# Kernel optimization log

Measured on AMD Instinct MI355X. Metric: run time of the kernel, lower is better.

## Reference

```python
import jax, jax.numpy as jnp
import numpy as np

D_K = 64  # per-head dim; source hardcodes d_k for the 1/sqrt(d_k) scale


def setup_inputs() -> dict:
    key = jax.random.key(0)
    kq, kk, kv = jax.random.split(key, 3)
    shape = (4, 16, 2048, D_K)  # [B, H, S, d]
    return {
        "q_s": jax.random.normal(kq, shape, dtype=jnp.float32),
        "k_s": jax.random.normal(kk, shape, dtype=jnp.float32),
        "v_s": jax.random.normal(kv, shape, dtype=jnp.float32),
    }


def reference(q_s, k_s, v_s):
    # scores = Q K^T / sqrt(d_k)  -> [B, H, S, S] (full matrix, unfused, as in source)
    scale = 1.0 / jnp.sqrt(jnp.asarray(D_K, dtype=q_s.dtype))
    scores = jnp.einsum("bhqd,bhkd->bhqk", q_s, k_s) * scale
    attn = jax.nn.softmax(scores, axis=-1)
    # out = attn @ V -> [B, H, S, d]
    return jnp.einsum("bhqk,bhkd->bhqd", attn, v_s)
```

## Files before the change

### kernel.cpp

```cpp
#include <hip/hip_runtime.h>
#include <stdint.h>
#include <math.h>

#define S_LEN 2048
#define DIM   64
#define QBLK  128
#define KVBLK 32
#define NKV   (S_LEN / KVBLK)

typedef __attribute__((ext_vector_type(8))) short short8;
typedef __attribute__((ext_vector_type(4))) float f32x4;

static __device__ __forceinline__ unsigned short f2bf(float f) {
    union { float f; uint32_t u; } cv; cv.f = f;
    uint32_t u = cv.u;
    return (unsigned short)((u + 0x7fffu + ((u >> 16) & 1u)) >> 16);
}

static __device__ __forceinline__ void gload16(const void* g, void* l) {
    __builtin_amdgcn_global_load_lds(
        (const __attribute__((address_space(1))) unsigned int*)g,
        (__attribute__((address_space(3))) unsigned int*)l, 16, 0, 0);
}

static __device__ __forceinline__ float vmax3(float a, float b, float c) {
    float d;
    asm("v_max3_f32 %0, %1, %2, %3" : "=v"(d) : "v"(a), "v"(b), "v"(c));
    return d;
}

__global__ void cvt_k(const float* __restrict__ kp, unsigned short* __restrict__ kws) {
    const int idx = blockIdx.x * 256 + threadIdx.x;
    const int c   = idx & 7;
    const int s   = (idx >> 3) & (S_LEN - 1);
    const int bh  = idx >> 14;
    const float* src = kp + ((size_t)bh * S_LEN + s) * DIM + c * 8;
    const f32x4 a = *reinterpret_cast<const f32x4*>(src);
    const f32x4 b = *reinterpret_cast<const f32x4*>(src + 4);
    short8 t;
    t[0] = (short)f2bf(a[0]); t[1] = (short)f2bf(a[1]);
    t[2] = (short)f2bf(a[2]); t[3] = (short)f2bf(a[3]);
    t[4] = (short)f2bf(b[0]); t[5] = (short)f2bf(b[1]);
    t[6] = (short)f2bf(b[2]); t[7] = (short)f2bf(b[3]);
    unsigned short* dst = kws + ((size_t)bh * S_LEN + s) * DIM + (size_t)((c ^ (s & 7)) * 8);
    *reinterpret_cast<short8*>(dst) = t;
}

__global__ void cvt_v(const float* __restrict__ vp, unsigned short* __restrict__ vtws) {
    const int bh = blockIdx.x >> 5;
    const int T  = blockIdx.x & 31;
    const int tid = threadIdx.x;
    __shared__ unsigned short ldsT[DIM][72];

    const int i = tid >> 2;
    const int dbase = (tid & 3) * 16;
    const float* src = vp + ((size_t)bh * S_LEN + T * 64 + i) * DIM + dbase;
#pragma unroll
    for (int q4 = 0; q4 < 4; ++q4) {
        const f32x4 a = *reinterpret_cast<const f32x4*>(src + q4 * 4);
#pragma unroll
        for (int j = 0; j < 4; ++j) ldsT[dbase + q4 * 4 + j][i] = f2bf(a[j]);
    }
    __syncthreads();
#pragma unroll
    for (int hh = 0; hh < 2; ++hh) {
        const int slot = tid + hh * 256;
        const int d = slot >> 3;
        const int h = (slot >> 2) & 1;
        const int c_st = slot & 3;
        const int cl = c_st ^ ((d >> 1) & 3);
        short8 t8;
#pragma unroll
        for (int j = 0; j < 8; ++j) {
            const int p = cl * 8 + j;
            const int kap = ((p & 4) << 2) | ((p & 16) >> 1) | ((p & 8) >> 1) | (p & 3);
            t8[j] = (short)ldsT[d][h * 32 + kap];
        }
        unsigned short* dst = vtws + ((size_t)bh * DIM + d) * S_LEN + T * 64 + h * 32 + c_st * 8;
        *reinterpret_cast<short8*>(dst) = t8;
    }
}

#define QK_TILE(ST, KL)                                                                               \
    do {                                                                                              \
        __builtin_amdgcn_s_setprio(1);                                                                \
        _Pragma("unroll")                                                                             \
        for (int nt = 0; nt < 2; ++nt) {                                                              \
            const short8 kf0 = *reinterpret_cast<const short8*>((KL) + koff[nt][0]);                  \
            const short8 kf1 = *reinterpret_cast<const short8*>((KL) + koff[nt][1]);                  \
            ST[0][nt] = __builtin_amdgcn_mfma_f32_16x16x32_bf16(kf0, qfrag[0][0], z4, 0, 0, 0);       \
            ST[1][nt] = __builtin_amdgcn_mfma_f32_16x16x32_bf16(kf0, qfrag[1][0], z4, 0, 0, 0);       \
            ST[0][nt] = __builtin_amdgcn_mfma_f32_16x16x32_bf16(kf1, qfrag[0][1], ST[0][nt], 0, 0, 0);\
            ST[1][nt] = __builtin_amdgcn_mfma_f32_16x16x32_bf16(kf1, qfrag[1][1], ST[1][nt], 0, 0, 0);\
        }                                                                                             \
        __builtin_amdgcn_s_setprio(0);                                                                \
    } while (0)

#define SMPV(ST, VL)                                                                                  \
    do {                                                                                              \
        short8 pfA, pfB;                                                                              \
        _Pragma("unroll")                                                                             \
        for (int mt = 0; mt < 2; ++mt) {                                                              \
            const f32x4 s0 = ST[mt][0], s1 = ST[mt][1];                                               \
            const float a0 = vmax3(s0[0], s0[1], s0[2]);                                              \
            const float a1 = vmax3(s0[3], s1[0], s1[1]);                                              \
            const float lane_mx = vmax3(a0, a1, fmaxf(s1[2], s1[3]));                                 \
            if (__any(lane_mx > m_run[mt] + 8.0f)) {                                                  \
                float mx = fmaxf(lane_mx, __shfl_xor(lane_mx, 16));                                   \
                mx = fmaxf(mx, __shfl_xor(mx, 32));                                                   \
                const float mnew = fmaxf(m_run[mt], mx);                                              \
                const float al = __builtin_amdgcn_exp2f(m_run[mt] - mnew);                            \
                m_run[mt] = mnew;                                                                     \
                l_part[mt] *= al;                                                                     \
                _Pragma("unroll")                                                                     \
                for (int nt = 0; nt < 4; ++nt) {                                                      \
                    f32x4 sc = o[mt][nt];                                                             \
                    sc[0] *= al; sc[1] *= al; sc[2] *= al; sc[3] *= al;                               \
                    o[mt][nt] = sc;                                                                   \
                }                                                                                     \
            }                                                                                         \
            const float mnow = m_run[mt];                                                             \
            f32x4 p0, p1;                                                                             \
            p0[0] = __builtin_amdgcn_exp2f(ST[mt][0][0] - mnow);                                      \
            p0[1] = __builtin_amdgcn_exp2f(ST[mt][0][1] - mnow);                                      \
            p0[2] = __builtin_amdgcn_exp2f(ST[mt][0][2] - mnow);                                      \
            p0[3] = __builtin_amdgcn_exp2f(ST[mt][0][3] - mnow);                                      \
            p1[0] = __builtin_amdgcn_exp2f(ST[mt][1][0] - mnow);                                      \
            p1[1] = __builtin_amdgcn_exp2f(ST[mt][1][1] - mnow);                                      \
            p1[2] = __builtin_amdgcn_exp2f(ST[mt][1][2] - mnow);                                      \
            p1[3] = __builtin_amdgcn_exp2f(ST[mt][1][3] - mnow);                                      \
            l_part[mt] += ((p0[0] + p0[1]) + (p0[2] + p0[3])) + ((p1[0] + p1[1]) + (p1[2] + p1[3])); \
            union { uint32_t u[4]; short8 v; } fr;                                                    \
            asm("v_cvt_pk_bf16_f32 %0, %1, %2" : "=v"(fr.u[0]) : "v"(p0[0]), "v"(p0[1]));             \
            asm("v_cvt_pk_bf16_f32 %0, %1, %2" : "=v"(fr.u[1]) : "v"(p0[2]), "v"(p0[3]));             \
            asm("v_cvt_pk_bf16_f32 %0, %1, %2" : "=v"(fr.u[2]) : "v"(p1[0]), "v"(p1[1]));             \
            asm("v_cvt_pk_bf16_f32 %0, %1, %2" : "=v"(fr.u[3]) : "v"(p1[2]), "v"(p1[3]));             \
            if (mt == 0) pfA = fr.v; else pfB = fr.v;                                                 \
        }                                                                                             \
        __builtin_amdgcn_s_setprio(1);                                                                \
        _Pragma("unroll")                                                                             \
        for (int ntd = 0; ntd < 4; ++ntd) {                                                           \
            const short8 vf = *reinterpret_cast<const short8*>((VL) + voff[ntd]);                     \
            o[0][ntd] = __builtin_amdgcn_mfma_f32_16x16x32_bf16(vf, pfA, o[0][ntd], 0, 0, 0);         \
            o[1][ntd] = __builtin_amdgcn_mfma_f32_16x16x32_bf16(vf, pfB, o[1][ntd], 0, 0, 0);         \
        }                                                                                             \
        __builtin_amdgcn_s_setprio(0);                                                                \
    } while (0)

__global__ __launch_bounds__(256, 4)
void attn_fwd(const float* __restrict__ qp, const unsigned short* __restrict__ kws,
              const unsigned short* __restrict__ vtws, float* __restrict__ op) {
    const int lb = (blockIdx.x & 7) * 128 + (blockIdx.x >> 3);
    const int bh = lb >> 4;
    const int qb = lb & 15;
    const int tid  = threadIdx.x;
    const int wave = tid >> 6;
    const int lane = tid & 63;
    const int g = lane >> 4;
    const int r = lane & 15;

    __shared__ unsigned short klds[2][KVBLK * DIM];
    __shared__ unsigned short vlds[2][DIM * 32];

    const float*          qg    = qp   + (size_t)bh * (S_LEN * DIM);
    const unsigned short* kbase = kws  + (size_t)bh * (S_LEN * DIM);
    const unsigned short* vbase = vtws + (size_t)bh * (S_LEN * DIM);
    float*                og    = op   + (size_t)bh * (S_LEN * DIM);

    const float qscale = 0.125f * 1.44269504088896340736f;
    const int q0 = qb * QBLK + wave * 32;
    short8 qfrag[2][2];
#pragma unroll
    for (int mt = 0; mt < 2; ++mt) {
        const float* qrow = qg + (size_t)(q0 + mt * 16 + r) * DIM;
#pragma unroll
        for (int ks = 0; ks < 2; ++ks) {
            const f32x4 a = *reinterpret_cast<const f32x4*>(qrow + ks * 32 + 8 * g);
            const f32x4 b = *reinterpret_cast<const f32x4*>(qrow + ks * 32 + 8 * g + 4);
            short8 t;
            t[0] = (short)f2bf(a[0] * qscale); t[1] = (short)f2bf(a[1] * qscale);
            t[2] = (short)f2bf(a[2] * qscale); t[3] = (short)f2bf(a[3] * qscale);
            t[4] = (short)f2bf(b[0] * qscale); t[5] = (short)f2bf(b[1] * qscale);
            t[6] = (short)f2bf(b[2] * qscale); t[7] = (short)f2bf(b[3] * qscale);
            qfrag[mt][ks] = t;
        }
    }

    f32x4 o[2][4];
    float m_run[2], l_part[2];
#pragma unroll
    for (int mt = 0; mt < 2; ++mt) {
#pragma unroll
        for (int nt = 0; nt < 4; ++nt) { f32x4 z = {0.f, 0.f, 0.f, 0.f}; o[mt][nt] = z; }
        m_run[mt] = -INFINITY; l_part[mt] = 0.0f;
    }

    const int srow = lane >> 3, schk = lane & 7;
    const int vd = wave * 16 + ((lane >> 2) & 15), vcst = lane & 3;
    auto stageK = [&](int t, int buf) {
        gload16(kbase + (size_t)(t * KVBLK + wave * 8 + srow) * DIM + schk * 8,
                &klds[buf][(wave * 8) * DIM]);
    };
    auto stageV = [&](int t, int buf) {
        gload16(vbase + (size_t)vd * S_LEN + (t >> 1) * 64 + (t & 1) * 32 + vcst * 8,
                &vlds[buf][wave * 512]);
    };

    int koff[2][2], voff[4];
#pragma unroll
    for (int nt = 0; nt < 2; ++nt)
#pragma unroll
        for (int ks = 0; ks < 2; ++ks)
            koff[nt][ks] = (nt * 16 + r) * DIM + (((ks << 2) | g) ^ (r & 7)) * 8;
#pragma unroll
    for (int nt = 0; nt < 4; ++nt)
        voff[nt] = (nt * 16 + r) * 32 + (g ^ ((r >> 1) & 3)) * 8;

    const f32x4 z4 = {0.f, 0.f, 0.f, 0.f};
    const unsigned short* kl0 = &klds[0][0];
    const unsigned short* kl1 = &klds[1][0];
    const unsigned short* vl0 = &vlds[0][0];
    const unsigned short* vl1 = &vlds[1][0];

    f32x4 stA[2][2], stB[2][2];

    stageK(0, 0);
    __syncthreads();
    stageK(1, 1); stageV(0, 0);
    QK_TILE(stA, kl0);
    __syncthreads();
    stageK(2, 0); stageV(1, 1);
    QK_TILE(stB, kl1);
    SMPV(stA, vl0);
    __syncthreads();

    for (int tt = 2; tt < NKV; tt += 2) {
        stageK(tt + 1, 1);
        stageV(tt, 0);
        QK_TILE(stA, kl0);
        SMPV(stB, vl1);
        __syncthreads();
        if (tt + 2 < NKV) stageK(tt + 2, 0);
        stageV(tt + 1, 1);
        QK_TILE(stB, kl1);
        SMPV(stA, vl0);
        __syncthreads();
    }
    SMPV(stB, vl1);

#pragma unroll
    for (int mt = 0; mt < 2; ++mt) {
        float lfull = l_part[mt];
        lfull += __shfl_xor(lfull, 16);
        lfull += __shfl_xor(lfull, 32);
        const float inv = 1.0f / lfull;
        float* dst = og + (size_t)(q0 + mt * 16 + r) * DIM + 4 * g;
#pragma unroll
        for (int ntd = 0; ntd < 4; ++ntd) {
            f32x4 tt = o[mt][ntd];
            tt[0] *= inv; tt[1] *= inv; tt[2] *= inv; tt[3] *= inv;
            *reinterpret_cast<f32x4*>(dst + ntd * 16) = tt;
        }
    }
}

extern "C" void kernel_launch(void* const* d_in, const int* in_sizes, int n_in,
                              void* d_out, int out_size, void* d_ws, size_t ws_size,
                              hipStream_t stream) {
    const float* q = (const float*)d_in[0];
    const float* k = (const float*)d_in[1];
    const float* v = (const float*)d_in[2];
    float* out = (float*)d_out;
    unsigned short* kws  = (unsigned short*)d_ws;
    unsigned short* vtws = kws + (size_t)64 * S_LEN * DIM;
    cvt_k<<<dim3(64 * S_LEN * 8 / 256), 256, 0, stream>>>(k, kws);
    cvt_v<<<dim3(64 * (S_LEN / 64)), 256, 0, stream>>>(v, vtws);
    attn_fwd<<<dim3(1024), 256, 0, stream>>>(q, kws, vtws, out);
}
```

Before: 106.8 us.

## Use triple-buffered K/V staging with explicit vmcnt-gated barriers

Replaces the double-buffered K/V LDS scheme, which staggered QK and softmax-PV across two tiles, with a three-slot ring buffer. Each tile's K and V are loaded together two iterations ahead, and each barrier waits only until the oldest loads land via an explicit s_waitcnt vmcnt. This aims to hide global-to-LDS latency better and cut barriers to one per tile. In exchange it drops the software overlap between QK of one tile and PV of the previous, serialising QK and softmax-PV within an iteration. It also raises LDS use by half, which could affect occupancy.

```diff
diff --git a/kernel.cpp b/kernel.cpp
--- a/kernel.cpp
+++ b/kernel.cpp
@@ -147,6 +147,13 @@
         __builtin_amdgcn_s_setprio(0);                                                                \
     } while (0)
 
+#define PIPE_BARRIER(N)                                                                               \
+    do {                                                                                              \
+        asm volatile("s_waitcnt vmcnt(" #N ")" ::: "memory");                                         \
+        __builtin_amdgcn_s_barrier();                                                                 \
+        __builtin_amdgcn_sched_barrier(0);                                                            \
+    } while (0)
+
 __global__ __launch_bounds__(256, 4)
 void attn_fwd(const float* __restrict__ qp, const unsigned short* __restrict__ kws,
               const unsigned short* __restrict__ vtws, float* __restrict__ op) {
@@ -159,8 +166,8 @@
     const int g = lane >> 4;
     const int r = lane & 15;
 
-    __shared__ unsigned short klds[2][KVBLK * DIM];
-    __shared__ unsigned short vlds[2][DIM * 32];
+    __shared__ unsigned short klds[3 * KVBLK * DIM];
+    __shared__ unsigned short vlds[3 * DIM * 32];
 
     const float*          qg    = qp   + (size_t)bh * (S_LEN * DIM);
     const unsigned short* kbase = kws  + (size_t)bh * (S_LEN * DIM);
@@ -197,13 +204,11 @@
 
     const int srow = lane >> 3, schk = lane & 7;
     const int vd = wave * 16 + ((lane >> 2) & 15), vcst = lane & 3;
-    auto stageK = [&](int t, int buf) {
+    auto stage = [&](int t, int buf_off) {
         gload16(kbase + (size_t)(t * KVBLK + wave * 8 + srow) * DIM + schk * 8,
-                &klds[buf][(wave * 8) * DIM]);
-    };
-    auto stageV = [&](int t, int buf) {
+                &klds[buf_off + wave * 512]);
         gload16(vbase + (size_t)vd * S_LEN + (t >> 1) * 64 + (t & 1) * 32 + vcst * 8,
-                &vlds[buf][wave * 512]);
+                &vlds[buf_off + wave * 512]);
     };
 
     int koff[2][2], voff[4];
@@ -217,36 +222,27 @@
         voff[nt] = (nt * 16 + r) * 32 + (g ^ ((r >> 1) & 3)) * 8;
 
     const f32x4 z4 = {0.f, 0.f, 0.f, 0.f};
-    const unsigned short* kl0 = &klds[0][0];
-    const unsigned short* kl1 = &klds[1][0];
-    const unsigned short* vl0 = &vlds[0][0];
-    const unsigned short* vl1 = &vlds[1][0];
-
-    f32x4 stA[2][2], stB[2][2];
-
-    stageK(0, 0);
-    __syncthreads();
-    stageK(1, 1); stageV(0, 0);
-    QK_TILE(stA, kl0);
-    __syncthreads();
-    stageK(2, 0); stageV(1, 1);
-    QK_TILE(stB, kl1);
-    SMPV(stA, vl0);
-    __syncthreads();
-
-    for (int tt = 2; tt < NKV; tt += 2) {
-        stageK(tt + 1, 1);
-        stageV(tt, 0);
-        QK_TILE(stA, kl0);
-        SMPV(stB, vl1);
-        __syncthreads();
-        if (tt + 2 < NKV) stageK(tt + 2, 0);
-        stageV(tt + 1, 1);
-        QK_TILE(stB, kl1);
-        SMPV(stA, vl0);
-        __syncthreads();
-    }
-    SMPV(stB, vl1);
+    f32x4 st[2][2];
+
+    int offA = 0, offB = 2048, offC = 4096;
+
+    stage(0, offA);
+    stage(1, offB);
+    PIPE_BARRIER(2);
+
+    for (int t = 0; t < NKV - 2; ++t) {
+        stage(t + 2, offC);
+        QK_TILE(st, klds + offA);
+        SMPV(st, vlds + offA);
+        PIPE_BARRIER(2);
+        const int tmp = offA; offA = offB; offB = offC; offC = tmp;
+    }
+    QK_TILE(st, klds + offA);
+    SMPV(st, vlds + offA);
+    PIPE_BARRIER(0);
+    { const int tmp = offA; offA = offB; offB = offC; offC = tmp; }
+    QK_TILE(st, klds + offA);
+    SMPV(st, vlds + offA);
 
 #pragma unroll
     for (int mt = 0; mt < 2; ++mt) {
```

Result: slower. 111.3 us (+4.2%).
